# Kernel optimization log

Measured on AMD Instinct MI355X. Metric: run time of the kernel, lower is better.

The kernel has to match this reference:

```python
import jax, jax.numpy as jnp
import numpy as np

PAD_IDX = 0


def setup_inputs() -> dict:
    key = jax.random.key(0)
    ks = jax.random.split(key, 6)
    nentries, entry_size, bsize, nemb, vocab = 8000, 32, 64, 256, 50000
    keys = jax.random.randint(ks[0], (nentries,), 0, vocab)
    entries = jax.random.randint(ks[1], (nentries, entry_size), 0, vocab)
    query = jax.random.normal(ks[2], (bsize, nemb), dtype=jnp.float32)
    wordemb = jax.random.normal(ks[3], (vocab, nemb), dtype=jnp.float32)
    qproj_w = jax.random.uniform(ks[4], (nemb, nemb), jnp.float32, -0.1, 0.1)
    qproj_b = jnp.zeros((nemb,), jnp.float32)
    return dict(keys=keys, entries=entries, query=query, wordemb=wordemb,
                qproj_w=qproj_w, qproj_b=qproj_b)


def _embed(ids, wordemb):
    # F.embedding with padding_idx: gathered rows at pad_idx are zeroed
    return wordemb[ids] * (ids != PAD_IDX)[..., None].astype(wordemb.dtype)


def reference(keys, entries, query, wordemb, qproj_w, qproj_b):
    keys_e = _embed(keys, wordemb)       # (m, d)
    ents_e = _embed(entries, wordemb)    # (m, n, d)
    # --- single hop (max_hops = 1) ---
    # value_atten: query attends over the n tokens inside each entry
    vq = query @ qproj_w.T + qproj_b                       # (b, d)
    logits_v = jnp.einsum('ik,mnk->imn', vq, ents_e)       # (b, m, n)
    prob_v = jax.nn.softmax(logits_v, axis=-1)
    ents = jnp.einsum('imn,mnk->imk', prob_v, ents_e)      # (b, m, d)
    # entry_atten: query attends over entries via their keys
    logits_e = jnp.einsum('ik,jk->ij', query, keys_e)      # (b, m)
    prob_e = jax.nn.softmax(logits_e, axis=-1)
    o_k = prob_e @ keys_e                                  # (b, d)
    combined = jnp.einsum('bm,bme->be', prob_e, ents)      # (b, d)
    # return (us[-1], prob_list[-1], combined_entries)
    return o_k, logits_e, combined
```

## Files before the change

kernel.cpp:

```cpp
#include <hip/hip_runtime.h>
#include <math.h>

#define B 64
#define D 256
#define M 8000
#define N 32
#define LG_LD 8000
#define EPB 16
#define NBLK (M / EPB)
#define VOCAB 50000

typedef unsigned short u16;
typedef __bf16 bf16x8 __attribute__((ext_vector_type(8)));
typedef float fx4 __attribute__((ext_vector_type(4)));

#define STR_E  264
#define STR_P  40

static __device__ __forceinline__ u16 f2bf(float x) {
    unsigned int u = __float_as_uint(x);
    u += 0x7FFFu + ((u >> 16) & 1u);
    return (u16)(u >> 16);
}
static __device__ __forceinline__ float bf2f(u16 h) {
    return __uint_as_float(((unsigned)h) << 16);
}
static __device__ __forceinline__ uint4 pack8(float4 va, float4 vb, float msk) {
    unsigned p0 = (unsigned)f2bf(va.x * msk) | ((unsigned)f2bf(va.y * msk) << 16);
    unsigned p1 = (unsigned)f2bf(va.z * msk) | ((unsigned)f2bf(va.w * msk) << 16);
    unsigned p2 = (unsigned)f2bf(vb.x * msk) | ((unsigned)f2bf(vb.y * msk) << 16);
    unsigned p3 = (unsigned)f2bf(vb.z * msk) | ((unsigned)f2bf(vb.w * msk) << 16);
    return make_uint4(p0, p1, p2, p3);
}

#define BARRIER_LGKM() do {                                   \
    asm volatile("s_waitcnt lgkmcnt(0)" ::: "memory");        \
    __builtin_amdgcn_s_barrier();                             \
    asm volatile("" ::: "memory");                            \
} while (0)

__global__ __launch_bounds__(256) void k_prep_all(const int* __restrict__ keys,
                                                  const float* __restrict__ emb,
                                                  const float* __restrict__ q,
                                                  const float* __restrict__ W,
                                                  const float* __restrict__ bias,
                                                  u16* __restrict__ embb,
                                                  u16* __restrict__ qbf,
                                                  u16* __restrict__ keb,
                                                  u16* __restrict__ vqb) {
    __shared__ float qs[D];
    int t = threadIdx.x, bid = blockIdx.x;
    if (bid < 6250) {
        size_t idx = (size_t)bid * 2048 + (size_t)t * 8;
        float4 v0 = *(const float4*)(emb + idx);
        float4 v1 = *(const float4*)(emb + idx + 4);
        float msk = (idx < D) ? 0.f : 1.f;
        uint4 pk = pack8(v0, v1, msk);
        *(uint4*)(embb + idx) = pk;
    } else if (bid < 7250) {
        int c = (bid - 6250) * 256 + t;
        int j = c >> 5, sp = c & 31;
        int id = keys[j];
        const float* rp = emb + (size_t)id * D + sp * 8;
        float4 v0 = *(const float4*)rp;
        float4 v1 = *(const float4*)(rp + 4);
        float msk = (id != 0) ? 1.f : 0.f;
        uint4 pk = pack8(v0, v1, msk);
        *(uint4*)(keb + (size_t)j * D + sp * 8) = pk;
    } else if (bid < 7258) {
        size_t idx = (size_t)(bid - 7250) * 2048 + (size_t)t * 8;
        float4 v0 = *(const float4*)(q + idx);
        float4 v1 = *(const float4*)(q + idx + 4);
        uint4 pk = pack8(v0, v1, 1.f);
        *(uint4*)(qbf + idx) = pk;
    } else {
        int b = bid - 7258;
        qs[t] = q[b * D + t];
        __syncthreads();
        const float* wr = W + t * D;
        float acc = bias[t];
#pragma unroll 8
        for (int k = 0; k < D; k += 4) {
            float4 w4 = *(const float4*)(wr + k);
            acc += qs[k] * w4.x + qs[k + 1] * w4.y + qs[k + 2] * w4.z + qs[k + 3] * w4.w;
        }
        vqb[b * D + t] = f2bf(acc);
    }
}

__global__ __launch_bounds__(256, 2) void k_heavy_f(const int* __restrict__ entries,
                                                    const u16* __restrict__ embb,
                                                    const u16* __restrict__ vqb,
                                                    const u16* __restrict__ qbf,
                                                    const u16* __restrict__ keb,
                                                    float* __restrict__ lg,
                                                    u16* __restrict__ numCp,
                                                    u16* __restrict__ numKp,
                                                    float* __restrict__ mLp,
                                                    float* __restrict__ denLp) {
    __shared__ __align__(16) u16 sEu[2][N * STR_E];
    __shared__ __align__(16) u16 sETu[2][64 * 136];
    __shared__ __align__(16) u16 sPu[B * STR_P];
    __shared__ float sw[EPB][B];

    int t = threadIdx.x;
    int lane = t & 63, l = lane & 15, q = lane >> 4, w = t >> 6;
    int b0 = 16 * w;
    int sp = t & 31, n0 = t >> 5;
    int m0 = blockIdx.x * EPB;
    int bb = t & 63, y = t >> 6;
    int swzk = (sp >> 2) & 3;

    int idc[4], idn[4];
    uint4 pfF[4];
#pragma unroll
    for (int i = 0; i < 4; ++i) idc[i] = entries[m0 * N + n0 + 8 * i];
#pragma unroll
    for (int i = 0; i < 4; ++i)
        pfF[i] = *(const uint4*)(embb + (size_t)idc[i] * D + sp * 8);

    fx4 zero4 = {0.f, 0.f, 0.f, 0.f};
    fx4 aL = zero4;
#pragma unroll
    for (int s = 0; s < 8; ++s) {
        bf16x8 a  = *(const bf16x8*)(qbf + (size_t)(b0 + l) * D + 32 * s + 8 * q);
        bf16x8 bq = *(const bf16x8*)(keb + (size_t)(m0 + l) * D + 32 * s + 8 * q);
        aL = __builtin_amdgcn_mfma_f32_16x16x32_bf16(a, bq, aL, 0, 0, 0);
    }
#pragma unroll
    for (int r = 0; r < 4; ++r)
        lg[(size_t)(b0 + 4 * q + r) * LG_LD + m0 + l] = aL[r];

#pragma unroll
    for (int r = 0; r < 4; ++r) {
        float m_ = aL[r];
        m_ = fmaxf(m_, __shfl_xor(m_, 1));
        m_ = fmaxf(m_, __shfl_xor(m_, 2));
        m_ = fmaxf(m_, __shfl_xor(m_, 4));
        m_ = fmaxf(m_, __shfl_xor(m_, 8));
        float wv = __expf(aL[r] - m_);
        sw[l][b0 + 4 * q + r] = wv;
        float d_ = wv;
        d_ += __shfl_xor(d_, 1);
        d_ += __shfl_xor(d_, 2);
        d_ += __shfl_xor(d_, 4);
        d_ += __shfl_xor(d_, 8);
        if (l == 0) {
            mLp[blockIdx.x * B + b0 + 4 * q + r] = m_;
            denLp[blockIdx.x * B + b0 + 4 * q + r] = d_;
        }
    }

    bf16x8 vqf[8];
#pragma unroll
    for (int s = 0; s < 8; ++s)
        vqf[s] = *(const bf16x8*)(vqb + (b0 + l) * D + 32 * s + 8 * q);

    fx4 acc[16];
#pragma unroll
    for (int dt = 0; dt < 16; ++dt) acc[dt] = zero4;

    {
#pragma unroll
        for (int i = 0; i < 4; ++i)
            *(uint4*)&sEu[0][(n0 + 8 * i) * STR_E + sp * 8] = pfF[i];
#pragma unroll
        for (int j = 0; j < 8; ++j) {
            unsigned a0 = (((unsigned*)&pfF[0])[j >> 1] >> ((j & 1) * 16)) & 0xFFFFu;
            unsigned a1 = (((unsigned*)&pfF[1])[j >> 1] >> ((j & 1) * 16)) & 0xFFFFu;
            unsigned a2 = (((unsigned*)&pfF[2])[j >> 1] >> ((j & 1) * 16)) & 0xFFFFu;
            unsigned a3 = (((unsigned*)&pfF[3])[j >> 1] >> ((j & 1) * 16)) & 0xFFFFu;
            uint2 pr = make_uint2(a0 | (a1 << 16), a2 | (a3 << 16));
            int off = (2 * sp + (j >> 2)) * 136 + (j & 3) * 32 +
                      (((n0 >> 1) ^ swzk) << 3) + (n0 & 1) * 4;
            *(uint2*)&sETu[0][off] = pr;
        }
    }
#pragma unroll
    for (int i = 0; i < 4; ++i) idc[i] = entries[(m0 + 1) * N + n0 + 8 * i];
#pragma unroll
    for (int i = 0; i < 4; ++i)
        pfF[i] = *(const uint4*)(embb + (size_t)idc[i] * D + sp * 8);
#pragma unroll
    for (int i = 0; i < 4; ++i) idn[i] = entries[(m0 + 2) * N + n0 + 8 * i];

    int offL2 = (l >> 2) * 136 + (l & 3) * 32;

#pragma unroll 2
    for (int e = 0; e < EPB; ++e) {
        __syncthreads();
        int nxt = (e + 1) & 1;
        if (e < EPB - 1) {
#pragma unroll
            for (int i = 0; i < 4; ++i)
                *(uint4*)&sEu[nxt][(n0 + 8 * i) * STR_E + sp * 8] = pfF[i];
#pragma unroll
            for (int j = 0; j < 8; ++j) {
                unsigned a0 = (((unsigned*)&pfF[0])[j >> 1] >> ((j & 1) * 16)) & 0xFFFFu;
                unsigned a1 = (((unsigned*)&pfF[1])[j >> 1] >> ((j & 1) * 16)) & 0xFFFFu;
                unsigned a2 = (((unsigned*)&pfF[2])[j >> 1] >> ((j & 1) * 16)) & 0xFFFFu;
                unsigned a3 = (((unsigned*)&pfF[3])[j >> 1] >> ((j & 1) * 16)) & 0xFFFFu;
                uint2 pr = make_uint2(a0 | (a1 << 16), a2 | (a3 << 16));
                int off = (2 * sp + (j >> 2)) * 136 + (j & 3) * 32 +
                          (((n0 >> 1) ^ swzk) << 3) + (n0 & 1) * 4;
                *(uint2*)&sETu[nxt][off] = pr;
            }
            if (e < EPB - 2) {
#pragma unroll
                for (int i = 0; i < 4; ++i)
                    pfF[i] = *(const uint4*)(embb + (size_t)idn[i] * D + sp * 8);
#pragma unroll
                for (int i = 0; i < 4; ++i) idc[i] = idn[i];
                if (e < EPB - 3) {
#pragma unroll
                    for (int i = 0; i < 4; ++i) idn[i] = entries[(m0 + e + 3) * N + n0 + 8 * i];
                }
            }
        }
        int cur = e & 1;
        fx4 accS[2];
        accS[0] = zero4; accS[1] = zero4;
#pragma unroll
        for (int T = 0; T < 2; ++T)
#pragma unroll
            for (int s = 0; s < 8; ++s) {
                bf16x8 ea = *(const bf16x8*)&sEu[cur][(16 * T + l) * STR_E + 32 * s + 8 * q];
                accS[T] = __builtin_amdgcn_mfma_f32_16x16x32_bf16(ea, vqf[s], accS[T], 0, 0, 0);
            }
        float swb = sw[e][b0 + l];
        float mx = -INFINITY;
#pragma unroll
        for (int T = 0; T < 2; ++T)
#pragma unroll
            for (int r = 0; r < 4; ++r) mx = fmaxf(mx, accS[T][r]);
        mx = fmaxf(mx, __shfl_xor(mx, 16));
        mx = fmaxf(mx, __shfl_xor(mx, 32));
        float pe[2][4], sum = 0.f;
#pragma unroll
        for (int T = 0; T < 2; ++T)
#pragma unroll
            for (int r = 0; r < 4; ++r) {
                pe[T][r] = __expf(accS[T][r] - mx);
                sum += pe[T][r];
            }
        sum += __shfl_xor(sum, 16);
        sum += __shfl_xor(sum, 32);
        float sc = swb / sum;
#pragma unroll
        for (int T = 0; T < 2; ++T)
#pragma unroll
            for (int r = 0; r < 4; ++r) {
                int nn = 16 * T + 4 * q + r;
                int slot = 4 * (nn & 7) + (nn >> 3);
                sPu[(b0 + l) * STR_P + slot] = f2bf(pe[T][r] * sc);
            }
        BARRIER_LGKM();
        {
            bf16x8 paA[4];
#pragma unroll
            for (int bg = 0; bg < 4; ++bg)
                paA[bg] = *(const bf16x8*)&sPu[(16 * bg + l) * STR_P + 8 * q];
#pragma unroll
            for (int dtl = 0; dtl < 4; ++dtl) {
                int qs8 = (q ^ ((2 * w + (dtl >> 1)) & 3)) * 8;
                bf16x8 eb = *(const bf16x8*)&sETu[cur][offL2 + (4 * w + dtl) * 544 + qs8];
#pragma unroll
                for (int bg = 0; bg < 4; ++bg)
                    acc[4 * bg + dtl] = __builtin_amdgcn_mfma_f32_16x16x32_bf16(
                        paA[bg], eb, acc[4 * bg + dtl], 0, 0, 0);
            }
        }
    }

    u16* ncp = numCp + (size_t)blockIdx.x * (B * D);
#pragma unroll
    for (int bg = 0; bg < 4; ++bg)
#pragma unroll
        for (int dtl = 0; dtl < 4; ++dtl)
#pragma unroll
            for (int r = 0; r < 4; ++r)
                ncp[(16 * bg + 4 * q + r) * D + 16 * (4 * w + dtl) + l] =
                    f2bf(acc[4 * bg + dtl][r]);

    __syncthreads();
    {
        int rp = t >> 5;
        uint4 ka = *(const uint4*)(keb + (size_t)(m0 + rp) * D + sp * 8);
        uint4 kb = *(const uint4*)(keb + (size_t)(m0 + rp + 8) * D + sp * 8);
#pragma unroll
        for (int j = 0; j < 8; ++j) {
            unsigned a0 = (((unsigned*)&ka)[j >> 1] >> ((j & 1) * 16)) & 0xFFFFu;
            unsigned a1 = (((unsigned*)&kb)[j >> 1] >> ((j & 1) * 16)) & 0xFFFFu;
            int d = 8 * sp + j;
            int sl = 2 * rp;
            int off = (d >> 2) * 136 + (d & 3) * 32 +
                      ((((sl >> 3)) ^ swzk) << 3) + (sl & 7);
            *(unsigned*)&sETu[0][off] = a0 | (a1 << 16);
        }
#pragma unroll
        for (int i = 0; i < 4; ++i) {
            int m = 4 * i + y;
            int slot = 2 * (m & 7) + (m >> 3);
            sPu[bb * STR_P + slot] = f2bf(sw[m][bb]);
        }
        *(uint2*)&sPu[bb * STR_P + 16 + 4 * y] = make_uint2(0u, 0u);
    }
    __syncthreads();
    fx4 acc2[16];
#pragma unroll
    for (int dt = 0; dt < 16; ++dt) acc2[dt] = zero4;
    {
        bf16x8 pa2A[4];
#pragma unroll
        for (int bg = 0; bg < 4; ++bg)
            pa2A[bg] = *(const bf16x8*)&sPu[(16 * bg + l) * STR_P + 8 * q];
#pragma unroll
        for (int dtl = 0; dtl < 4; ++dtl) {
            int qs8 = (q ^ ((2 * w + (dtl >> 1)) & 3)) * 8;
            bf16x8 eb2 = *(const bf16x8*)&sETu[0][offL2 + (4 * w + dtl) * 544 + qs8];
#pragma unroll
            for (int bg = 0; bg < 4; ++bg)
                acc2[4 * bg + dtl] = __builtin_amdgcn_mfma_f32_16x16x32_bf16(
                    pa2A[bg], eb2, acc2[4 * bg + dtl], 0, 0, 0);
        }
    }
    u16* nkp = numKp + (size_t)blockIdx.x * (B * D);
#pragma unroll
    for (int bg = 0; bg < 4; ++bg)
#pragma unroll
        for (int dtl = 0; dtl < 4; ++dtl)
#pragma unroll
            for (int r = 0; r < 4; ++r)
                nkp[(16 * bg + 4 * q + r) * D + 16 * (4 * w + dtl) + l] =
                    f2bf(acc2[4 * bg + dtl][r]);
}

__global__ __launch_bounds__(256) void k_comb2(const u16* __restrict__ numCp,
                                               const u16* __restrict__ numKp,
                                               const float* __restrict__ mLp,
                                               const float* __restrict__ denLp,
                                               float* __restrict__ o_k,
                                               float* __restrict__ comb) {
    __shared__ float sscale[NBLK];
    __shared__ float red[256];
    __shared__ float sro[32][33], src[32][33];
    __shared__ float srden;
    int bid = blockIdx.x;
    int b = bid >> 3, d0 = (bid & 7) * 32;
    int t = threadIdx.x;
    float mx = -INFINITY;
    for (int blk = t; blk < NBLK; blk += 256) mx = fmaxf(mx, mLp[blk * B + b]);
    red[t] = mx;
    __syncthreads();
    for (int s = 128; s > 0; s >>= 1) {
        if (t < s) red[t] = fmaxf(red[t], red[t + s]);
        __syncthreads();
    }
    float Mg = red[0];
    __syncthreads();
    float ds = 0.f;
    for (int blk = t; blk < NBLK; blk += 256) {
        float sc = __expf(mLp[blk * B + b] - Mg);
        sscale[blk] = sc;
        ds += sc * denLp[blk * B + b];
    }
    red[t] = ds;
    __syncthreads();
    for (int s = 128; s > 0; s >>= 1) {
        if (t < s) red[t] += red[t + s];
        __syncthreads();
    }
    if (t == 0) srden = 1.f / red[0];
    __syncthreads();
    int v = t & 7, s = t >> 3;
    float ao[4] = {0.f, 0.f, 0.f, 0.f}, ac[4] = {0.f, 0.f, 0.f, 0.f};
    for (int blk = s; blk < NBLK; blk += 32) {
        float sc = sscale[blk];
        size_t i = (size_t)blk * (B * D) + (size_t)b * D + d0 + v * 4;
        uint2 kk = *(const uint2*)(numKp + i);
        uint2 cc = *(const uint2*)(numCp + i);
        ao[0] += sc * bf2f((u16)(kk.x & 0xFFFFu));
        ao[1] += sc * bf2f((u16)(kk.x >> 16));
        ao[2] += sc * bf2f((u16)(kk.y & 0xFFFFu));
        ao[3] += sc * bf2f((u16)(kk.y >> 16));
        ac[0] += sc * bf2f((u16)(cc.x & 0xFFFFu));
        ac[1] += sc * bf2f((u16)(cc.x >> 16));
        ac[2] += sc * bf2f((u16)(cc.y & 0xFFFFu));
        ac[3] += sc * bf2f((u16)(cc.y >> 16));
    }
#pragma unroll
    for (int k = 0; k < 4; ++k) {
        sro[s][v * 4 + k] = ao[k];
        src[s][v * 4 + k] = ac[k];
    }
    __syncthreads();
    if (t < 32) {
        float so = 0.f, sc2 = 0.f;
#pragma unroll
        for (int k2 = 0; k2 < 32; ++k2) { so += sro[k2][t]; sc2 += src[k2][t]; }
        float rd = srden;
        o_k[b * D + d0 + t] = so * rd;
        comb[b * D + d0 + t] = sc2 * rd;
    }
}


extern "C" void kernel_launch(void* const* d_in, const int* in_sizes, int n_in,
                              void* d_out, int out_size, void* d_ws, size_t ws_size,
                              hipStream_t stream) {
    const int*   keys    = (const int*)d_in[0];
    const int*   entries = (const int*)d_in[1];
    const float* query   = (const float*)d_in[2];
    const float* wordemb = (const float*)d_in[3];
    const float* qproj_w = (const float*)d_in[4];
    const float* qproj_b = (const float*)d_in[5];

    float* out  = (float*)d_out;
    float* o_k  = out;
    float* lg   = out + B * D;
    float* comb = out + B * D + B * M;

    char* wsb = (char*)d_ws;
    u16*   embb  = (u16*)wsb;
    u16*   keb   = (u16*)(wsb + 25600000);
    u16*   qbf   = (u16*)(wsb + 29696000);
    u16*   vqb   = (u16*)(wsb + 29728768);
    u16*   numCp = (u16*)(wsb + 29761536);
    u16*   numKp = (u16*)(wsb + 46145536);
    float* mLp   = (float*)(wsb + 62529536);
    float* denLp = (float*)(wsb + 62657536);

    k_prep_all<<<7322, 256, 0, stream>>>(keys, wordemb, query, qproj_w, qproj_b,
                                         embb, qbf, keb, vqb);
    k_heavy_f<<<NBLK, 256, 0, stream>>>(entries, embb, vqb, qbf, keb, lg,
                                        numCp, numKp, mLp, denLp);
    k_comb2<<<512, 256, 0, stream>>>(numCp, numKp, mLp, denLp, o_k, comb);
}
```

Before: 165.1 us.

## Double entries per block to halve partial outputs and combine work

Each heavy-kernel block now processes 32 entries instead of 16, which halves the grid and the number of per-block partial numerator and softmax-stat buffers written to workspace and later reduced. Entry-softmax logits are computed in two 16-row MFMA halves with a joint max. Weights are stored as bf16 in shared memory to save LDS, and the key-transpose and probability-staging code is reworked so the second MFMA stage uses the full K=32 instead of zero padding. The cost is a longer serial loop per block and fewer blocks to fill the GPU (250 instead of 500).

```diff
diff --git a/kernel.cpp b/kernel.cpp
--- a/kernel.cpp
+++ b/kernel.cpp
@@ -6,7 +6,7 @@
 #define M 8000
 #define N 32
 #define LG_LD 8000
-#define EPB 16
+#define EPB 32
 #define NBLK (M / EPB)
 #define VOCAB 50000
 
@@ -101,7 +101,7 @@
     __shared__ __align__(16) u16 sEu[2][N * STR_E];
     __shared__ __align__(16) u16 sETu[2][64 * 136];
     __shared__ __align__(16) u16 sPu[B * STR_P];
-    __shared__ float sw[EPB][B];
+    __shared__ u16 sw16[EPB][B];
 
     int t = threadIdx.x;
     int lane = t & 63, l = lane & 15, q = lane >> 4, w = t >> 6;
@@ -120,33 +120,46 @@
         pfF[i] = *(const uint4*)(embb + (size_t)idc[i] * D + sp * 8);
 
     fx4 zero4 = {0.f, 0.f, 0.f, 0.f};
-    fx4 aL = zero4;
-#pragma unroll
-    for (int s = 0; s < 8; ++s) {
-        bf16x8 a  = *(const bf16x8*)(qbf + (size_t)(b0 + l) * D + 32 * s + 8 * q);
-        bf16x8 bq = *(const bf16x8*)(keb + (size_t)(m0 + l) * D + 32 * s + 8 * q);
-        aL = __builtin_amdgcn_mfma_f32_16x16x32_bf16(a, bq, aL, 0, 0, 0);
-    }
-#pragma unroll
-    for (int r = 0; r < 4; ++r)
-        lg[(size_t)(b0 + 4 * q + r) * LG_LD + m0 + l] = aL[r];
+    fx4 aLg[2];
+#pragma unroll
+    for (int mh = 0; mh < 2; ++mh) {
+        fx4 aL = zero4;
+#pragma unroll
+        for (int s = 0; s < 8; ++s) {
+            bf16x8 a  = *(const bf16x8*)(qbf + (size_t)(b0 + l) * D + 32 * s + 8 * q);
+            bf16x8 bq = *(const bf16x8*)(keb + (size_t)(m0 + 16 * mh + l) * D + 32 * s + 8 * q);
+            aL = __builtin_amdgcn_mfma_f32_16x16x32_bf16(a, bq, aL, 0, 0, 0);
+        }
+        aLg[mh] = aL;
+#pragma unroll
+        for (int r = 0; r < 4; ++r)
+            lg[(size_t)(b0 + 4 * q + r) * LG_LD + m0 + 16 * mh + l] = aL[r];
+    }
 
 #pragma unroll
     for (int r = 0; r < 4; ++r) {
-        float m_ = aL[r];
-        m_ = fmaxf(m_, __shfl_xor(m_, 1));
-        m_ = fmaxf(m_, __shfl_xor(m_, 2));
-        m_ = fmaxf(m_, __shfl_xor(m_, 4));
-        m_ = fmaxf(m_, __shfl_xor(m_, 8));
-        float wv = __expf(aL[r] - m_);
-        sw[l][b0 + 4 * q + r] = wv;
-        float d_ = wv;
+        float m0_ = aLg[0][r];
+        m0_ = fmaxf(m0_, __shfl_xor(m0_, 1));
+        m0_ = fmaxf(m0_, __shfl_xor(m0_, 2));
+        m0_ = fmaxf(m0_, __shfl_xor(m0_, 4));
+        m0_ = fmaxf(m0_, __shfl_xor(m0_, 8));
+        float m1_ = aLg[1][r];
+        m1_ = fmaxf(m1_, __shfl_xor(m1_, 1));
+        m1_ = fmaxf(m1_, __shfl_xor(m1_, 2));
+        m1_ = fmaxf(m1_, __shfl_xor(m1_, 4));
+        m1_ = fmaxf(m1_, __shfl_xor(m1_, 8));
+        float mB = fmaxf(m0_, m1_);
+        float wv0 = __expf(aLg[0][r] - mB);
+        float wv1 = __expf(aLg[1][r] - mB);
+        sw16[l][b0 + 4 * q + r]      = f2bf(wv0);
+        sw16[16 + l][b0 + 4 * q + r] = f2bf(wv1);
+        float d_ = wv0 + wv1;
         d_ += __shfl_xor(d_, 1);
         d_ += __shfl_xor(d_, 2);
         d_ += __shfl_xor(d_, 4);
         d_ += __shfl_xor(d_, 8);
         if (l == 0) {
-            mLp[blockIdx.x * B + b0 + 4 * q + r] = m_;
+            mLp[blockIdx.x * B + b0 + 4 * q + r] = mB;
             denLp[blockIdx.x * B + b0 + 4 * q + r] = d_;
         }
     }
@@ -227,7 +240,7 @@
                 bf16x8 ea = *(const bf16x8*)&sEu[cur][(16 * T + l) * STR_E + 32 * s + 8 * q];
                 accS[T] = __builtin_amdgcn_mfma_f32_16x16x32_bf16(ea, vqf[s], accS[T], 0, 0, 0);
             }
-        float swb = sw[e][b0 + l];
+        float swb = bf2f(sw16[e][b0 + l]);
         float mx = -INFINITY;
 #pragma unroll
         for (int T = 0; T < 2; ++T)
@@ -284,26 +297,26 @@
 
     __syncthreads();
     {
-        int rp = t >> 5;
-        uint4 ka = *(const uint4*)(keb + (size_t)(m0 + rp) * D + sp * 8);
-        uint4 kb = *(const uint4*)(keb + (size_t)(m0 + rp + 8) * D + sp * 8);
+        uint4 kv[4];
+#pragma unroll
+        for (int i = 0; i < 4; ++i)
+            kv[i] = *(const uint4*)(keb + (size_t)(m0 + n0 + 8 * i) * D + sp * 8);
 #pragma unroll
         for (int j = 0; j < 8; ++j) {
-            unsigned a0 = (((unsigned*)&ka)[j >> 1] >> ((j & 1) * 16)) & 0xFFFFu;
-            unsigned a1 = (((unsigned*)&kb)[j >> 1] >> ((j & 1) * 16)) & 0xFFFFu;
-            int d = 8 * sp + j;
-            int sl = 2 * rp;
-            int off = (d >> 2) * 136 + (d & 3) * 32 +
-                      ((((sl >> 3)) ^ swzk) << 3) + (sl & 7);
-            *(unsigned*)&sETu[0][off] = a0 | (a1 << 16);
-        }
-#pragma unroll
-        for (int i = 0; i < 4; ++i) {
-            int m = 4 * i + y;
-            int slot = 2 * (m & 7) + (m >> 3);
-            sPu[bb * STR_P + slot] = f2bf(sw[m][bb]);
-        }
-        *(uint2*)&sPu[bb * STR_P + 16 + 4 * y] = make_uint2(0u, 0u);
+            unsigned a0 = (((unsigned*)&kv[0])[j >> 1] >> ((j & 1) * 16)) & 0xFFFFu;
+            unsigned a1 = (((unsigned*)&kv[1])[j >> 1] >> ((j & 1) * 16)) & 0xFFFFu;
+            unsigned a2 = (((unsigned*)&kv[2])[j >> 1] >> ((j & 1) * 16)) & 0xFFFFu;
+            unsigned a3 = (((unsigned*)&kv[3])[j >> 1] >> ((j & 1) * 16)) & 0xFFFFu;
+            uint2 pr = make_uint2(a0 | (a1 << 16), a2 | (a3 << 16));
+            int off = (2 * sp + (j >> 2)) * 136 + (j & 3) * 32 +
+                      (((n0 >> 1) ^ swzk) << 3) + (n0 & 1) * 4;
+            *(uint2*)&sETu[0][off] = pr;
+        }
+#pragma unroll
+        for (int j = 0; j < 8; ++j) {
+            int m = 8 * y + j;
+            sPu[bb * STR_P + 4 * j + y] = sw16[m][bb];
+        }
     }
     __syncthreads();
     fx4 acc2[16];
@@ -426,9 +439,9 @@
     u16*   qbf   = (u16*)(wsb + 29696000);
     u16*   vqb   = (u16*)(wsb + 29728768);
     u16*   numCp = (u16*)(wsb + 29761536);
-    u16*   numKp = (u16*)(wsb + 46145536);
-    float* mLp   = (float*)(wsb + 62529536);
-    float* denLp = (float*)(wsb + 62657536);
+    u16*   numKp = (u16*)(wsb + 37953536);
+    float* mLp   = (float*)(wsb + 46145536);
+    float* denLp = (float*)(wsb + 46209536);
 
     k_prep_all<<<7322, 256, 0, stream>>>(keys, wordemb, query, qproj_w, qproj_b,
                                          embb, qbf, keb, vqb);
```

Result: no change. 168.0 us (+1.7%).
